# Performance work log

Hardware: AMD Instinct MI355X
Metric: run time of the kernel (lower is better)

The kernel has to match this reference:

```python
import jax, jax.numpy as jnp
import numpy as np

R = 16
ALPHA = 16.0
SCALING = ALPHA / R  # = 1.0


def setup_inputs() -> dict:
    key = jax.random.key(0)
    k1, k2, k3 = jax.random.split(key, 3)
    x = jax.random.normal(k1, (4, 4096, 4096), dtype=jnp.float32)
    A = jax.random.normal(k2, (4096, R), dtype=jnp.float32)
    B = jax.random.normal(k3, (R, 4096), dtype=jnp.float32)
    return {"x": x, "A": A, "B": B}


def reference(x, A, B):
    # Faithful to torch: W_delta = A @ B * scaling; out = x @ W_delta
    # (dropout_p=0.0 so dropout is a no-op)
    W_delta = (A @ B) * SCALING  # [in, out]
    return jnp.matmul(x, W_delta)  # [b, s, out]
```

## Files before the change

kernel.cpp:

```cpp
#include <hip/hip_runtime.h>

constexpr int RANK = 16;
constexpr int K = 4096;
constexpr int N = 4096;
constexpr int M = 4 * 4096;
constexpr int KC = 512;
constexpr int NCHUNK = K / KC;
constexpr int ROWS2 = 32;


__global__ __launch_bounds__(256) void lora_xa(const float* __restrict__ x,
                                               const float* __restrict__ A,
                                               float* __restrict__ T) {
  const int lane = threadIdx.x & 63;
  const int tid = threadIdx.x;
  const int wave = tid >> 6;
  const int r0 = blockIdx.x * 16 + wave * 4;
  const int m = (lane >> 2) & 3;

  __shared__ float4 As[KC * 4];

  const float4* __restrict__ A4 = reinterpret_cast<const float4*>(A);

  float vals[64];
#pragma unroll
  for (int i = 0; i < 64; ++i) vals[i] = 0.0f;

  for (int c = 0; c < NCHUNK; ++c) {
    __syncthreads();
#pragma unroll
    for (int q = 0; q < 8; ++q) {
      const int n = q * 256 + tid;
      const int k = n >> 2;
      const int s = n & 3;
      const int p = s ^ ((k >> 2) & 3);
      As[k * 4 + p] = A4[(size_t)(c * KC + k) * 4 + s];
    }
    __syncthreads();

#pragma unroll
    for (int kbi = 0; kbi < 8; ++kbi) {
      const int kl = kbi * 64 + lane;
      const size_t kg = (size_t)c * KC + kl;

      float xv[4];
#pragma unroll
      for (int r = 0; r < 4; ++r) xv[r] = x[(size_t)(r0 + r) * K + kg];

      float4 a[4];
#pragma unroll
      for (int s = 0; s < 4; ++s) a[s] = As[kl * 4 + (s ^ m)];

#pragma unroll
      for (int r = 0; r < 4; ++r) {
#pragma unroll
        for (int s = 0; s < 4; ++s) {
          vals[r * 16 + 4 * s + 0] = fmaf(xv[r], a[s].x, vals[r * 16 + 4 * s + 0]);
          vals[r * 16 + 4 * s + 1] = fmaf(xv[r], a[s].y, vals[r * 16 + 4 * s + 1]);
          vals[r * 16 + 4 * s + 2] = fmaf(xv[r], a[s].z, vals[r * 16 + 4 * s + 2]);
          vals[r * 16 + 4 * s + 3] = fmaf(xv[r], a[s].w, vals[r * 16 + 4 * s + 3]);
        }
      }
    }
  }

#define RSTEP(HALF)                                            \
  {                                                            \
    const bool hi = (lane & (HALF)) != 0;                      \
    _Pragma("unroll")                                          \
    for (int i = 0; i < (HALF); ++i) {                         \
      const float send = hi ? vals[i] : vals[i + (HALF)];      \
      const float keep = hi ? vals[i + (HALF)] : vals[i];      \
      vals[i] = keep + __shfl_xor(send, (HALF), 64);           \
    }                                                          \
  }
  RSTEP(32)
  RSTEP(16)
  RSTEP(8)
  RSTEP(4)
  RSTEP(2)
  RSTEP(1)
#undef RSTEP

  T[(size_t)(r0 + (lane >> 4)) * RANK + (lane & 15)] = vals[0];
}

__global__ __launch_bounds__(256) void lora_tb(const float* __restrict__ T,
                                               const float* __restrict__ B,
                                               float* __restrict__ out) {
  const int n0 = blockIdx.x * 1024 + threadIdx.x * 4;
  const int r0 = blockIdx.y * ROWS2;

  const float4* __restrict__ B4 = reinterpret_cast<const float4*>(B);
  float4* __restrict__ out4 = reinterpret_cast<float4*>(out);

  float4 b[16];
#pragma unroll
  for (int j = 0; j < RANK; ++j) b[j] = B4[((size_t)j * N + n0) >> 2];

  for (int r = 0; r < ROWS2; ++r) {
    const float* __restrict__ t = T + (size_t)(r0 + r) * RANK;
    float4 acc;
    acc.x = acc.y = acc.z = acc.w = 0.0f;
#pragma unroll
    for (int j = 0; j < RANK; ++j) {
      const float ts = t[j];
      acc.x = fmaf(ts, b[j].x, acc.x);
      acc.y = fmaf(ts, b[j].y, acc.y);
      acc.z = fmaf(ts, b[j].z, acc.z);
      acc.w = fmaf(ts, b[j].w, acc.w);
    }
    out4[((size_t)(r0 + r) * N + n0) >> 2] = acc;
  }
}

extern "C" void kernel_launch(void* const* d_in, const int* in_sizes, int n_in,
                              void* d_out, int out_size, void* d_ws, size_t ws_size,
                              hipStream_t stream) {
  const float* x = (const float*)d_in[0];
  const float* A = (const float*)d_in[1];
  const float* B = (const float*)d_in[2];
  float* out = (float*)d_out;
  float* T = (float*)d_ws;

  lora_xa<<<M / 16, 256, 0, stream>>>(x, A, T);

  lora_tb<<<dim3(N / 1024, M / ROWS2), 256, 0, stream>>>(T, B, out);
}
```

Measured before the change: 133.2 us.

## Restructure x@A kernel with float4 x loads and transposed swizzled A tile

Reworks the low-rank projection kernel. Each wave now handles 2 rows instead of 4 and reads x as float4 vectors, with smaller blocks of 8 rows and 256-wide K chunks. A is stored transposed and XOR-swizzled in shared memory so each lane reads one float4 per rank. Fewer accumulator registers (32 vs 64) should raise occupancy and widen x loads. The cost is that A is reloaded into shared memory more often per row, and the final shuffle reduction leaves half the lanes idle.

```diff
diff --git a/kernel.cpp b/kernel.cpp
--- a/kernel.cpp
+++ b/kernel.cpp
@@ -4,85 +4,89 @@
 constexpr int K = 4096;
 constexpr int N = 4096;
 constexpr int M = 4 * 4096;
-constexpr int KC = 512;
+constexpr int KC = 256;
 constexpr int NCHUNK = K / KC;
+constexpr int ROWSB = 8;
 constexpr int ROWS2 = 32;
 
 
 __global__ __launch_bounds__(256) void lora_xa(const float* __restrict__ x,
                                                const float* __restrict__ A,
                                                float* __restrict__ T) {
-  const int lane = threadIdx.x & 63;
   const int tid = threadIdx.x;
+  const int lane = tid & 63;
   const int wave = tid >> 6;
-  const int r0 = blockIdx.x * 16 + wave * 4;
-  const int m = (lane >> 2) & 3;
+  const int r0 = blockIdx.x * ROWSB + wave * 2;
 
-  __shared__ float4 As[KC * 4];
+  __shared__ float AsT[RANK][KC];
+  float4* __restrict__ AsT4 = reinterpret_cast<float4*>(&AsT[0][0]);
 
   const float4* __restrict__ A4 = reinterpret_cast<const float4*>(A);
+  const float4* __restrict__ x4 = reinterpret_cast<const float4*>(x);
 
-  float vals[64];
+  float vals[32];
 #pragma unroll
-  for (int i = 0; i < 64; ++i) vals[i] = 0.0f;
+  for (int i = 0; i < 32; ++i) vals[i] = 0.0f;
 
   for (int c = 0; c < NCHUNK; ++c) {
     __syncthreads();
 #pragma unroll
-    for (int q = 0; q < 8; ++q) {
+    for (int q = 0; q < 4; ++q) {
       const int n = q * 256 + tid;
       const int k = n >> 2;
       const int s = n & 3;
-      const int p = s ^ ((k >> 2) & 3);
-      As[k * 4 + p] = A4[(size_t)(c * KC + k) * 4 + s];
+      const float4 v = A4[c * 1024 + n];
+      const int kp = k ^ (s << 2);
+      AsT[4 * s + 0][kp] = v.x;
+      AsT[4 * s + 1][kp] = v.y;
+      AsT[4 * s + 2][kp] = v.z;
+      AsT[4 * s + 3][kp] = v.w;
     }
     __syncthreads();
 
-#pragma unroll
-    for (int kbi = 0; kbi < 8; ++kbi) {
-      const int kl = kbi * 64 + lane;
-      const size_t kg = (size_t)c * KC + kl;
-
-      float xv[4];
-#pragma unroll
-      for (int r = 0; r < 4; ++r) xv[r] = x[(size_t)(r0 + r) * K + kg];
-
-      float4 a[4];
-#pragma unroll
-      for (int s = 0; s < 4; ++s) a[s] = As[kl * 4 + (s ^ m)];
+    const float4 xv0 = x4[(size_t)(r0 + 0) * (K / 4) + c * (KC / 4) + lane];
+    const float4 xv1 = x4[(size_t)(r0 + 1) * (K / 4) + c * (KC / 4) + lane];
 
 #pragma unroll
-      for (int r = 0; r < 4; ++r) {
-#pragma unroll
-        for (int s = 0; s < 4; ++s) {
-          vals[r * 16 + 4 * s + 0] = fmaf(xv[r], a[s].x, vals[r * 16 + 4 * s + 0]);
-          vals[r * 16 + 4 * s + 1] = fmaf(xv[r], a[s].y, vals[r * 16 + 4 * s + 1]);
-          vals[r * 16 + 4 * s + 2] = fmaf(xv[r], a[s].z, vals[r * 16 + 4 * s + 2]);
-          vals[r * 16 + 4 * s + 3] = fmaf(xv[r], a[s].w, vals[r * 16 + 4 * s + 3]);
-        }
-      }
+    for (int j = 0; j < RANK; ++j) {
+      const float4 a = AsT4[j * (KC / 4) + (lane ^ (j >> 2))];
+      float acc0 = vals[j];
+      float acc1 = vals[16 + j];
+      acc0 = fmaf(xv0.x, a.x, acc0);
+      acc0 = fmaf(xv0.y, a.y, acc0);
+      acc0 = fmaf(xv0.z, a.z, acc0);
+      acc0 = fmaf(xv0.w, a.w, acc0);
+      acc1 = fmaf(xv1.x, a.x, acc1);
+      acc1 = fmaf(xv1.y, a.y, acc1);
+      acc1 = fmaf(xv1.z, a.z, acc1);
+      acc1 = fmaf(xv1.w, a.w, acc1);
+      vals[j] = acc0;
+      vals[16 + j] = acc1;
     }
   }
 
-#define RSTEP(HALF)                                            \
+#define FOLD(AH, LB)                                           \
   {                                                            \
-    const bool hi = (lane & (HALF)) != 0;                      \
+    const bool hi = (lane & (LB)) != 0;                        \
     _Pragma("unroll")                                          \
-    for (int i = 0; i < (HALF); ++i) {                         \
-      const float send = hi ? vals[i] : vals[i + (HALF)];      \
-      const float keep = hi ? vals[i + (HALF)] : vals[i];      \
-      vals[i] = keep + __shfl_xor(send, (HALF), 64);           \
+    for (int i = 0; i < (AH); ++i) {                           \
+      const float send = hi ? vals[i] : vals[i + (AH)];        \
+      const float keep = hi ? vals[i + (AH)] : vals[i];        \
+      vals[i] = keep + __shfl_xor(send, (LB), 64);             \
     }                                                          \
   }
-  RSTEP(32)
-  RSTEP(16)
-  RSTEP(8)
-  RSTEP(4)
-  RSTEP(2)
-  RSTEP(1)
-#undef RSTEP
+  FOLD(16, 32)
+  FOLD(8, 16)
+  FOLD(4, 8)
+  FOLD(2, 4)
+  FOLD(1, 2)
+#undef FOLD
+  vals[0] += __shfl_xor(vals[0], 1, 64);
 
-  T[(size_t)(r0 + (lane >> 4)) * RANK + (lane & 15)] = vals[0];
+  if (!(lane & 1)) {
+    const int e = lane >> 1;
+    T[(size_t)(r0 + (e >> 4)) * RANK + (e & 15)] = vals[0];
+  }
 }
 
 __global__ __launch_bounds__(256) void lora_tb(const float* __restrict__ T,
@@ -123,7 +127,7 @@
   float* out = (float*)d_out;
   float* T = (float*)d_ws;
 
-  lora_xa<<<M / 16, 256, 0, stream>>>(x, A, T);
+  lora_xa<<<M / ROWSB, 256, 0, stream>>>(x, A, T);
 
   lora_tb<<<dim3(N / 1024, M / ROWS2), 256, 0, stream>>>(T, B, out);
 }
```

New measurement: 148.7 us. 1.12x slower.

## Fuse x@A and T@B LoRA stages into a single kernel via shared memory

Applied to the files above, without the earlier changes.

Merges the two kernels so each block computes its 16 rows of T = x@A, keeps them in shared memory, and immediately writes the matching 16 rows of out = T@B across all columns. This removes the second launch and the global round trip of T. In exchange, each block reloads B for every 16-row tile and now writes the whole 16x4096 output slab itself. That changes the occupancy and the overlap between the read-heavy and write-heavy phases.

```diff
diff --git a/kernel.cpp b/kernel.cpp
--- a/kernel.cpp
+++ b/kernel.cpp
@@ -6,19 +6,19 @@
 constexpr int M = 4 * 4096;
 constexpr int KC = 512;
 constexpr int NCHUNK = K / KC;
-constexpr int ROWS2 = 32;
 
-
-__global__ __launch_bounds__(256) void lora_xa(const float* __restrict__ x,
-                                               const float* __restrict__ A,
-                                               float* __restrict__ T) {
+__global__ __launch_bounds__(256) void lora_fused(const float* __restrict__ x,
+                                                  const float* __restrict__ A,
+                                                  const float* __restrict__ B,
+                                                  float* __restrict__ out) {
   const int lane = threadIdx.x & 63;
   const int tid = threadIdx.x;
   const int wave = tid >> 6;
-  const int r0 = blockIdx.x * 16 + wave * 4;
-  const int m = (lane >> 2) & 3;
+  const int rbase = blockIdx.x * 16;
+  const int r0 = rbase + wave * 4;
 
   __shared__ float4 As[KC * 4];
+  __shared__ float Ts[16][RANK];
 
   const float4* __restrict__ A4 = reinterpret_cast<const float4*>(A);
 
@@ -34,10 +34,11 @@
       const int k = n >> 2;
       const int s = n & 3;
       const int p = s ^ ((k >> 2) & 3);
-      As[k * 4 + p] = A4[(size_t)(c * KC + k) * 4 + s];
+      As[k * 4 + p] = A4[(size_t)c * 2048 + n];
     }
     __syncthreads();
 
+    const int m = (lane >> 2) & 3;
 #pragma unroll
     for (int kbi = 0; kbi < 8; ++kbi) {
       const int kl = kbi * 64 + lane;
@@ -82,36 +83,45 @@
   RSTEP(1)
 #undef RSTEP
 
-  T[(size_t)(r0 + (lane >> 4)) * RANK + (lane & 15)] = vals[0];
-}
+  Ts[wave * 4 + (lane >> 4)][lane & 15] = vals[0];
+  __syncthreads();
 
-__global__ __launch_bounds__(256) void lora_tb(const float* __restrict__ T,
-                                               const float* __restrict__ B,
-                                               float* __restrict__ out) {
-  const int n0 = blockIdx.x * 1024 + threadIdx.x * 4;
-  const int r0 = blockIdx.y * ROWS2;
-
+  const int n0 = wave * 1024 + lane * 4;
   const float4* __restrict__ B4 = reinterpret_cast<const float4*>(B);
   float4* __restrict__ out4 = reinterpret_cast<float4*>(out);
 
-  float4 b[16];
+#pragma unroll 1
+  for (int cc = 0; cc < 4; ++cc) {
+    const int col = wave * 1024 + cc * 256 + lane * 4;
+
+    float4 b[16];
 #pragma unroll
-  for (int j = 0; j < RANK; ++j) b[j] = B4[((size_t)j * N + n0) >> 2];
+    for (int j = 0; j < RANK; ++j) b[j] = B4[((size_t)j * N + col) >> 2];
 
-  for (int r = 0; r < ROWS2; ++r) {
-    const float* __restrict__ t = T + (size_t)(r0 + r) * RANK;
-    float4 acc;
-    acc.x = acc.y = acc.z = acc.w = 0.0f;
+#pragma unroll 1
+    for (int r = 0; r < 16; ++r) {
+      const float4* __restrict__ tr4 =
+          reinterpret_cast<const float4*>(&Ts[r][0]);
+      const float4 t0 = tr4[0];
+      const float4 t1 = tr4[1];
+      const float4 t2 = tr4[2];
+      const float4 t3 = tr4[3];
+
+      float4 acc;
+      acc.x = acc.y = acc.z = acc.w = 0.0f;
+      const float tsv[16] = {t0.x, t0.y, t0.z, t0.w, t1.x, t1.y, t1.z, t1.w,
+                             t2.x, t2.y, t2.z, t2.w, t3.x, t3.y, t3.z, t3.w};
 #pragma unroll
-    for (int j = 0; j < RANK; ++j) {
-      const float ts = t[j];
-      acc.x = fmaf(ts, b[j].x, acc.x);
-      acc.y = fmaf(ts, b[j].y, acc.y);
-      acc.z = fmaf(ts, b[j].z, acc.z);
-      acc.w = fmaf(ts, b[j].w, acc.w);
+      for (int j = 0; j < RANK; ++j) {
+        acc.x = fmaf(tsv[j], b[j].x, acc.x);
+        acc.y = fmaf(tsv[j], b[j].y, acc.y);
+        acc.z = fmaf(tsv[j], b[j].z, acc.z);
+        acc.w = fmaf(tsv[j], b[j].w, acc.w);
+      }
+      out4[((size_t)(rbase + r) * N + col) >> 2] = acc;
     }
-    out4[((size_t)(r0 + r) * N + n0) >> 2] = acc;
   }
+  (void)n0;
 }
 
 extern "C" void kernel_launch(void* const* d_in, const int* in_sizes, int n_in,
@@ -121,9 +131,7 @@
   const float* A = (const float*)d_in[1];
   const float* B = (const float*)d_in[2];
   float* out = (float*)d_out;
-  float* T = (float*)d_ws;
+  (void)d_ws; (void)ws_size;
 
-  lora_xa<<<M / 16, 256, 0, stream>>>(x, A, T);
-
-  lora_tb<<<dim3(N / 1024, M / ROWS2), 256, 0, stream>>>(T, B, out);
+  lora_fused<<<M / 16, 256, 0, stream>>>(x, A, B, out);
 }
```

Result: faster. 129.7 us (-2.7%).
